# Kernel optimization log

Measured on AMD Instinct MI355X. Metric: run time of the kernel, lower is better.

## Reference

```python
import jax, jax.numpy as jnp
import numpy as np

NUM_HEADS = 8
EPS = 1e-12  # torch F.normalize default eps


def _l2norm(t):
    # t / max(||t||_2, eps) along last axis (matches F.normalize)
    n = jnp.sqrt(jnp.sum(t * t, axis=-1, keepdims=True))
    return t / jnp.maximum(n, EPS)


def setup_inputs() -> dict:
    key = jax.random.key(0)
    k1, k2, k3 = jax.random.split(key, 3)
    B, N, C = 8, 1024, 768
    x = jax.random.normal(k1, (B, N, C), dtype=jnp.float32)
    w_qkv = jax.random.normal(k2, (C, 3 * C), dtype=jnp.float32) * 0.02
    temperature = jnp.ones((NUM_HEADS, 1, 1), dtype=jnp.float32)
    w_proj = jax.random.normal(k3, (C, C), dtype=jnp.float32) * 0.02
    b_proj = jnp.zeros((C,), dtype=jnp.float32)
    return {"x": x, "w_qkv": w_qkv, "temperature": temperature,
            "w_proj": w_proj, "b_proj": b_proj}


def reference(x, w_qkv, temperature, w_proj, b_proj):
    B, N, C = x.shape
    H = NUM_HEADS
    hd = C // H
    # qkv projection (no bias), split into q,k,v of shape [B,H,N,hd]
    qkv = (x @ w_qkv).reshape(B, N, 3, H, hd)
    qkv = jnp.transpose(qkv, (2, 0, 3, 1, 4))  # [3,B,H,N,hd]
    q, k, v = qkv[0], qkv[1], qkv[2]
    q = _l2norm(q)
    k = _l2norm(k)
    # NOTE: code (unlike canonical XCA) does NOT transpose q/k, so attn is [B,H,N,N]
    attn = jnp.einsum('bhnd,bhmd->bhnm', q, k) * temperature  # temp broadcasts over B
    attn = jax.nn.softmax(attn, axis=-1)
    out = jnp.einsum('bhnm,bhmd->bhnd', attn, v)  # [B,H,N,hd]
    out = jnp.transpose(out, (0, 2, 1, 3)).reshape(B, N, C)
    return out @ w_proj + b_proj
```

## Files before the change

### kernel.cpp

```cpp
#include <hip/hip_runtime.h>
#include <math.h>

typedef __attribute__((ext_vector_type(8))) short bf16x8;
typedef __attribute__((ext_vector_type(4))) float f32x4;
typedef __attribute__((ext_vector_type(4))) unsigned int u32x4;
typedef unsigned short u16;
typedef unsigned int u32;


__device__ __forceinline__ u16 f2b(float f) {
  u32 u = __float_as_uint(f);
  return (u16)((u + 0x7fffu + ((u >> 16) & 1u)) >> 16);
}
__device__ __forceinline__ float b2f(u16 h) {
  return __uint_as_float(((u32)h) << 16);
}
__device__ __forceinline__ int swz(int m) { return (m ^ (m >> 2)) & 3; }

__device__ __forceinline__ void async16(const void* g, void* l) {
  __builtin_amdgcn_global_load_lds((const __attribute__((address_space(1))) u32*)g,
                                   (__attribute__((address_space(3))) u32*)l, 16, 0, 0);
}

template<int N> __device__ __forceinline__ void wait_vmcnt();
template<> __device__ __forceinline__ void wait_vmcnt<0>() {
  asm volatile("s_waitcnt vmcnt(0)" ::: "memory");
}
template<> __device__ __forceinline__ void wait_vmcnt<3>() {
  asm volatile("s_waitcnt vmcnt(3)" ::: "memory");
}

__global__ __launch_bounds__(256) void prep_kernel(const float* __restrict__ x,
                                                   const float* __restrict__ w_qkv,
                                                   const float* __restrict__ w_proj,
                                                   u16* __restrict__ xb,
                                                   u16* __restrict__ wqkvT,
                                                   u16* __restrict__ wprojT) {
  __shared__ float t[32][33];
  const int blk = blockIdx.x;
  if (blk < 6144) {
    const int idx = blk * 256 + threadIdx.x;
    const float4 v = ((const float4*)x)[idx];
    uint2 o;
    o.x = (u32)f2b(v.x) | ((u32)f2b(v.y) << 16);
    o.y = (u32)f2b(v.z) | ((u32)f2b(v.w) << 16);
    ((uint2*)xb)[idx] = o;
    return;
  }
  const float* in; u16* out; int R, C, bx, by;
  if (blk < 6144 + 1728) {
    const int rem = blk - 6144;
    in = w_qkv; out = wqkvT; R = 768; C = 2304; bx = rem % 72; by = rem / 72;
  } else {
    const int rem = blk - 6144 - 1728;
    in = w_proj; out = wprojT; R = 768; C = 768; bx = rem % 24; by = rem / 24;
  }
  const int c0 = bx * 32, r0 = by * 32;
  const int tc = threadIdx.x & 31, tr = threadIdx.x >> 5;
#pragma unroll
  for (int j = 0; j < 4; ++j)
    t[tr + j * 8][tc] = in[(size_t)(r0 + tr + j * 8) * C + c0 + tc];
  __syncthreads();
#pragma unroll
  for (int j = 0; j < 4; ++j)
    out[(size_t)(c0 + tr + j * 8) * R + r0 + tc] = f2b(t[tc][tr + j * 8]);
}

template<int NT>
__device__ __forceinline__ void gemm_core_bk64(const u16* __restrict__ A,
                                               const u16* __restrict__ Bt,
                                               int m0, int n0, f32x4 acc[4][NT / 32]) {
  constexpr int JT = NT / 32;
  constexpr int NG = (128 + NT) * 8;
  constexpr int NINST = NG / 256;
  __shared__ u16 Sm[2 * NG * 8];
  const int tid = threadIdx.x;
  const int w = tid >> 6, lane = tid & 63;
  const int i15 = lane & 15, quad = lane >> 4;
  const int wm = (w >> 1) * 64, wn = (w & 1) * (NT / 2);
  const int sw = quad ^ swz(i15);
  const int par = i15 & 1;

#pragma unroll
  for (int i = 0; i < 4; ++i)
#pragma unroll
    for (int j = 0; j < JT; ++j) acc[i][j] = (f32x4){0.f, 0.f, 0.f, 0.f};

  const u16* gsrc[NINST];
#pragma unroll
  for (int inst = 0; inst < NINST; ++inst) {
    const int s = inst * 256 + tid;
    if (s < 1024) {
      const int m = s >> 3, hp = (s >> 2) & 1, qd = s & 3;
      const int e = (hp ^ (m & 1)) * 4 + (qd ^ swz(m));
      gsrc[inst] = A + ((size_t)(m0 + m) * 768 + e * 8);
    } else {
      const int s2 = s - 1024;
      const int n = s2 >> 3, hp = (s2 >> 2) & 1, qd = s2 & 3;
      const int e = (hp ^ (n & 1)) * 4 + (qd ^ swz(n));
      gsrc[inst] = Bt + ((size_t)(n0 + n) * 768 + e * 8);
    }
  }

  auto stage = [&](int bsel) {
#pragma unroll
    for (int inst = 0; inst < NINST; ++inst) {
      async16(gsrc[inst], (void*)(Sm + ((size_t)bsel * NG + inst * 256 + w * 64) * 8));
      gsrc[inst] += 64;
    }
  };

  stage(0);

  for (int t = 0; t < 12; ++t) {
    __syncthreads();
    if (t < 11) stage((t + 1) & 1);
    const u16* buf = Sm + (size_t)(t & 1) * NG * 8;
#pragma unroll
    for (int kk = 0; kk < 2; ++kk) {
      bf16x8 af[4], bf[JT];
#pragma unroll
      for (int i = 0; i < 4; ++i) {
        const int mh = wm + i * 16 + i15;
        af[i] = *(const bf16x8*)(buf + ((size_t)mh * 8 + ((kk ^ par) << 2) + sw) * 8);
      }
#pragma unroll
      for (int j = 0; j < JT; ++j) {
        const int nh = wn + j * 16 + i15;
        bf[j] = *(const bf16x8*)(buf + ((size_t)1024 + nh * 8 + ((kk ^ par) << 2) + sw) * 8);
      }
#pragma unroll
      for (int i = 0; i < 4; ++i)
#pragma unroll
        for (int j = 0; j < JT; ++j)
          acc[i][j] = __builtin_amdgcn_mfma_f32_16x16x32_bf16(af[i], bf[j], acc[i][j], 0, 0, 0);
    }
  }
}

template<int NT>
__device__ __forceinline__ void gemm_core_c3(const u16* __restrict__ A,
                                             const u16* __restrict__ Bt,
                                             int m0, int n0, f32x4 acc[4][NT / 32]) {
  constexpr int JT = NT / 32;
  constexpr int NG = 512 + NT * 4;
  constexpr int NINST = NG / 256;
  __shared__ u16 Sm[3 * NG * 8];
  const int tid = threadIdx.x;
  const int w = tid >> 6, lane = tid & 63;
  const int i15 = lane & 15, quad = lane >> 4;
  const int wm = (w >> 1) * 64, wn = (w & 1) * (NT / 2);
  const int sw = quad ^ swz(i15);

#pragma unroll
  for (int i = 0; i < 4; ++i)
#pragma unroll
    for (int j = 0; j < JT; ++j) acc[i][j] = (f32x4){0.f, 0.f, 0.f, 0.f};

  const u16* gsrc[NINST];
#pragma unroll
  for (int inst = 0; inst < NINST; ++inst) {
    const int s = inst * 256 + tid;
    if (s < 512) {
      const int m = s >> 2, e = s & 3;
      gsrc[inst] = A + ((size_t)(m0 + m) * 768 + (e ^ swz(m)) * 8);
    } else {
      const int s2 = s - 512;
      const int n = s2 >> 2, e = s2 & 3;
      gsrc[inst] = Bt + ((size_t)(n0 + n) * 768 + (e ^ swz(n)) * 8);
    }
  }

  auto stage = [&](int bsel) {
#pragma unroll
    for (int inst = 0; inst < NINST; ++inst) {
      async16(gsrc[inst], (void*)(Sm + ((size_t)bsel * NG + inst * 256 + w * 64) * 8));
      gsrc[inst] += 32;
    }
  };

  stage(0);
  stage(1);

  for (int t = 0; t < 24; ++t) {
    if (t < 23) wait_vmcnt<NINST>();
    else        wait_vmcnt<0>();
    __builtin_amdgcn_s_barrier();
    __builtin_amdgcn_sched_barrier(0);
    if (t < 22) stage((t + 2) % 3);
    const u16* buf = Sm + (size_t)(t % 3) * NG * 8;
    bf16x8 af[4], bf[JT];
#pragma unroll
    for (int i = 0; i < 4; ++i)
      af[i] = *(const bf16x8*)(buf + ((size_t)(wm + i * 16 + i15) * 4 + sw) * 8);
#pragma unroll
    for (int j = 0; j < JT; ++j)
      bf[j] = *(const bf16x8*)(buf + ((size_t)512 + (wn + j * 16 + i15) * 4 + sw) * 8);
#pragma unroll
    for (int i = 0; i < 4; ++i)
#pragma unroll
      for (int j = 0; j < JT; ++j)
        acc[i][j] = __builtin_amdgcn_mfma_f32_16x16x32_bf16(af[i], bf[j], acc[i][j], 0, 0, 0);
  }
}

__global__ __launch_bounds__(256, 2) void qkv_gemm_kernel(
    const u16* __restrict__ xb, const u16* __restrict__ wT,
    const float* __restrict__ temp,
    u16* __restrict__ q, u16* __restrict__ k, u16* __restrict__ vT) {
  f32x4 acc[4][6];
  const int bid = blockIdx.x;
  const int xcd = bid & 7, slot = bid >> 3;
  const int mb = xcd * 8 + slot / 12, nb = slot % 12;
  const int m0 = mb * 128, n0 = nb * 192;
  gemm_core_bk64<192>(xb, wT, m0, n0, acc);

  const int tid = threadIdx.x, w = tid >> 6, lane = tid & 63;
  const int i15 = lane & 15, quad = lane >> 4;
  const int wm = (w >> 1) * 64;
  const int three = nb >> 2;
  const int h = ((nb & 3) << 1) + (w & 1);

  if (three < 2) {
    u16* dst = three ? k : q;
    const float sc_extra = three ? 1.f : temp[h];
#pragma unroll
    for (int it = 0; it < 4; ++it) {
#pragma unroll
      for (int r = 0; r < 4; ++r) {
        float s = 0.f;
#pragma unroll
        for (int jt = 0; jt < 6; ++jt) s += acc[it][jt][r] * acc[it][jt][r];
        s += __shfl_xor(s, 1); s += __shfl_xor(s, 2);
        s += __shfl_xor(s, 4); s += __shfl_xor(s, 8);
        const float scale = sc_extra / fmaxf(sqrtf(s), 1e-12f);
        const int m = m0 + wm + it * 16 + quad * 4 + r;
        const int b = m >> 10, n = m & 1023;
        u16* rowp = dst + ((size_t)(b * 8 + h) * 1024 + n) * 96;
#pragma unroll
        for (int jt = 0; jt < 6; ++jt)
          rowp[jt * 16 + i15] = f2b(acc[it][jt][r] * scale);
      }
    }
  } else {
#pragma unroll
    for (int it = 0; it < 4; ++it) {
      const int mb4 = m0 + wm + it * 16 + quad * 4;
      const int b = mb4 >> 10, nbase = mb4 & 1023;
#pragma unroll
      for (int jt = 0; jt < 6; ++jt) {
        const int d = jt * 16 + i15;
        uint2 pk;
        pk.x = (u32)f2b(acc[it][jt][0]) | ((u32)f2b(acc[it][jt][1]) << 16);
        pk.y = (u32)f2b(acc[it][jt][2]) | ((u32)f2b(acc[it][jt][3]) << 16);
        *(uint2*)(vT + ((size_t)(b * 8 + h) * 96 + d) * 1024 + nbase) = pk;
      }
    }
  }
}

__global__ __launch_bounds__(512, 4) void attn_kernel(
    const u16* __restrict__ q, const u16* __restrict__ kk,
    const u16* __restrict__ vT, u16* __restrict__ ctx) {
  __shared__ u16 smem[32768];
  const int tid = threadIdx.x, w = tid >> 6, lane = tid & 63;
  const int i15 = lane & 15, quad = lane >> 4;
  const int xs = swz(i15);
  const int bh = blockIdx.x & 63, qbase = (blockIdx.x >> 6) * 128;
  const int b = bh >> 3, h = bh & 7;
  u16* Pw = smem + 24576 + w * 1024;

  bf16x8 qf[3];
  {
    const int qrow = qbase + w * 16 + i15;
    const u16* qp = q + ((size_t)bh * 1024 + qrow) * 96 + quad * 8;
#pragma unroll
    for (int c = 0; c < 3; ++c) qf[c] = *(const bf16x8*)(qp + c * 32);
  }

  const u16* gsrc[3]; int gstep[3];
#pragma unroll
  for (int inst = 0; inst < 3; ++inst) {
    const int s = inst * 512 + tid;
    if (s < 768) {
      const int key6 = (s & 255) >> 2, c = s >> 8;
      const int e = c * 4 + ((s & 3) ^ swz(key6));
      gsrc[inst] = kk + ((size_t)bh * 1024 + key6) * 96 + e * 8;
      gstep[inst] = 64 * 96;
    } else {
      const int s2 = s - 768, r = s2 >> 2;
      const int c2 = (r >= 96), d = r - 96 * c2;
      gsrc[inst] = vT + ((size_t)bh * 96 + d) * 1024 + c2 * 32 + ((s2 & 3) ^ swz(d)) * 8;
      gstep[inst] = 64;
    }
  }

#pragma unroll
  for (int inst = 0; inst < 3; ++inst)
    async16(gsrc[inst], (void*)(smem + (size_t)(inst * 512 + w * 64) * 8));

  f32x4 o[6];
#pragma unroll
  for (int dt = 0; dt < 6; ++dt) o[dt] = (f32x4){0.f, 0.f, 0.f, 0.f};
  float l = 0.f;

  for (int t = 0; t < 16; ++t) {
    __syncthreads();
    const u16* KVs = smem + (t & 1) * 12288;
    if (t < 15) {
      u16* dst = smem + ((t + 1) & 1) * 12288;
#pragma unroll
      for (int inst = 0; inst < 3; ++inst) {
        gsrc[inst] += gstep[inst];
        async16(gsrc[inst], (void*)(dst + (size_t)(inst * 512 + w * 64) * 8));
      }
    }
#pragma unroll
    for (int kt = 0; kt < 4; ++kt) {
      bf16x8 af[3];
#pragma unroll
      for (int c = 0; c < 3; ++c)
        af[c] = *(const bf16x8*)(KVs + ((size_t)((c * 64 + kt * 16 + i15) * 4) + (quad ^ xs)) * 8);
      f32x4 s = (f32x4){0.f, 0.f, 0.f, 0.f};
#pragma unroll
      for (int c = 0; c < 3; ++c)
        s = __builtin_amdgcn_mfma_f32_16x16x32_bf16(af[c], qf[c], s, 0, 0, 0);
      const float e0 = __expf(s[0]), e1 = __expf(s[1]);
      const float e2 = __expf(s[2]), e3 = __expf(s[3]);
      l += (e0 + e1) + (e2 + e3);
      uint2 pk;
      pk.x = (u32)f2b(e0) | ((u32)f2b(e1) << 16);
      pk.y = (u32)f2b(e2) | ((u32)f2b(e3) << 16);
      const int pg = (kt & 1) * 2 + (quad >> 1);
      *(uint2*)(Pw + (size_t)(((kt >> 1) * 16 + i15) * 4 + (pg ^ xs)) * 8
                    + (quad & 1) * 4) = pk;
    }
#pragma unroll
    for (int c2 = 0; c2 < 2; ++c2) {
      const bf16x8 pa = *(const bf16x8*)(Pw + (size_t)((c2 * 16 + i15) * 4 + (quad ^ xs)) * 8);
#pragma unroll
      for (int dt = 0; dt < 6; ++dt) {
        const bf16x8 vb = *(const bf16x8*)(KVs +
            ((size_t)(768 + (c2 * 96 + dt * 16 + i15) * 4) + (quad ^ xs)) * 8);
        o[dt] = __builtin_amdgcn_mfma_f32_16x16x32_bf16(pa, vb, o[dt], 0, 0, 0);
      }
    }
  }

  l += __shfl_xor(l, 16); l += __shfl_xor(l, 32);
  __syncthreads();
  u16* scr = smem + w * 1664;
#pragma unroll
  for (int r = 0; r < 4; ++r) {
    const float linv = 1.f / __shfl(l, quad * 4 + r);
    const int row16 = quad * 4 + r;
#pragma unroll
    for (int dt = 0; dt < 6; ++dt)
      scr[row16 * 104 + dt * 16 + i15] = f2b(o[dt][r] * linv);
  }
#pragma unroll
  for (int jj = 0; jj < 3; ++jj) {
    const int id = jj * 64 + lane;
    const int row16 = id / 12, g = id - row16 * 12;
    const int grow = b * 1024 + qbase + w * 16 + row16;
    *(uint4*)(ctx + (size_t)grow * 768 + h * 96 + g * 8) =
        *(const uint4*)(scr + row16 * 104 + g * 8);
  }
}

__global__ __launch_bounds__(256, 4) void proj_gemm_kernel(
    const u16* __restrict__ ctx, const u16* __restrict__ wT,
    const float* __restrict__ bias, float* __restrict__ out) {
  f32x4 acc[4][2];
  const int bid = blockIdx.x;
  const int xcd = bid & 7, slot = bid >> 3;
  const int mb = xcd * 8 + slot / 12, nb = slot % 12;
  const int m0 = mb * 128, n0 = nb * 64;
  gemm_core_c3<64>(ctx, wT, m0, n0, acc);

  const int tid = threadIdx.x, w = tid >> 6, lane = tid & 63;
  const int i15 = lane & 15, quad = lane >> 4;
  const int wm = (w >> 1) * 64, wn = (w & 1) * 32;
#pragma unroll
  for (int jt = 0; jt < 2; ++jt) {
    const int c = n0 + wn + jt * 16 + i15;
    const float bb = bias[c];
#pragma unroll
    for (int it = 0; it < 4; ++it) {
#pragma unroll
      for (int r = 0; r < 4; ++r) {
        const int m = m0 + wm + it * 16 + quad * 4 + r;
        out[(size_t)m * 768 + c] = acc[it][jt][r] + bb;
      }
    }
  }
}

extern "C" void kernel_launch(void* const* d_in, const int* in_sizes, int n_in,
                              void* d_out, int out_size, void* d_ws, size_t ws_size,
                              hipStream_t stream) {
  const float* x      = (const float*)d_in[0];
  const float* w_qkv  = (const float*)d_in[1];
  const float* temp   = (const float*)d_in[2];
  const float* w_proj = (const float*)d_in[3];
  const float* b_proj = (const float*)d_in[4];

  u16* ws      = (u16*)d_ws;
  u16* xb      = ws;
  u16* wqkvT   = xb + 6291456;
  u16* qb      = wqkvT + 1769472;
  u16* kb      = qb + 6291456;
  u16* vTb     = kb + 6291456;
  u16* ctxb    = vTb + 6291456;
  u16* wprojT  = ctxb + 6291456;

  prep_kernel<<<8448, 256, 0, stream>>>(x, w_qkv, w_proj, xb, wqkvT, wprojT);
  qkv_gemm_kernel<<<768, 256, 0, stream>>>(xb, wqkvT, temp, qb, kb, vTb);
  attn_kernel<<<512, 512, 0, stream>>>(qb, kb, vTb, ctxb);
  proj_gemm_kernel<<<768, 256, 0, stream>>>(ctxb, wprojT, b_proj, (float*)d_out);
}
```

Measured before the change: 178.3 us.

## Use single-buffered BK32 QKV GEMM, raise occupancy, add setprio and intrinsic bf16 convert

Replaces the double-buffered BK=64 QKV GEMM core with a single-buffered BK=32 loop that issues async loads and syncs twice per iteration. Launch bounds for the QKV kernel rise from 2 to 3 blocks per CU, trading software pipelining for more resident waves. The attention kernel wraps its MFMA groups in s_setprio and swaps the manual bf16 rounding for the HIP intrinsic conversion. Losing overlap of loads with MFMA inside a block may stall the GEMM unless the extra occupancy hides that latency.

```diff
diff --git a/kernel.cpp b/kernel.cpp
--- a/kernel.cpp
+++ b/kernel.cpp
@@ -1,4 +1,5 @@
 #include <hip/hip_runtime.h>
+#include <hip/hip_bf16.h>
 #include <math.h>
 
 typedef __attribute__((ext_vector_type(8))) short bf16x8;
@@ -11,6 +12,10 @@
 __device__ __forceinline__ u16 f2b(float f) {
   u32 u = __float_as_uint(f);
   return (u16)((u + 0x7fffu + ((u >> 16) & 1u)) >> 16);
+}
+__device__ __forceinline__ u16 f2bq(float f) {
+  __hip_bfloat16 h = __float2bfloat16(f);
+  return __bfloat16_as_ushort(h);
 }
 __device__ __forceinline__ float b2f(u16 h) {
   return __uint_as_float(((u32)h) << 16);
@@ -67,74 +72,52 @@
 }
 
 template<int NT>
-__device__ __forceinline__ void gemm_core_bk64(const u16* __restrict__ A,
-                                               const u16* __restrict__ Bt,
-                                               int m0, int n0, f32x4 acc[4][NT / 32]) {
+__device__ __forceinline__ void gemm_core2b(const u16* __restrict__ A,
+                                            const u16* __restrict__ Bt,
+                                            int m0, int n0, f32x4 acc[4][NT / 32]) {
   constexpr int JT = NT / 32;
-  constexpr int NG = (128 + NT) * 8;
-  constexpr int NINST = NG / 256;
-  __shared__ u16 Sm[2 * NG * 8];
+  constexpr int NINST = (512 + NT * 4) / 256;
+  __shared__ u16 Sm[(512 + NT * 4) * 8];
   const int tid = threadIdx.x;
   const int w = tid >> 6, lane = tid & 63;
   const int i15 = lane & 15, quad = lane >> 4;
   const int wm = (w >> 1) * 64, wn = (w & 1) * (NT / 2);
   const int sw = quad ^ swz(i15);
-  const int par = i15 & 1;
 
 #pragma unroll
   for (int i = 0; i < 4; ++i)
 #pragma unroll
     for (int j = 0; j < JT; ++j) acc[i][j] = (f32x4){0.f, 0.f, 0.f, 0.f};
 
-  const u16* gsrc[NINST];
-#pragma unroll
-  for (int inst = 0; inst < NINST; ++inst) {
-    const int s = inst * 256 + tid;
-    if (s < 1024) {
-      const int m = s >> 3, hp = (s >> 2) & 1, qd = s & 3;
-      const int e = (hp ^ (m & 1)) * 4 + (qd ^ swz(m));
-      gsrc[inst] = A + ((size_t)(m0 + m) * 768 + e * 8);
-    } else {
-      const int s2 = s - 1024;
-      const int n = s2 >> 3, hp = (s2 >> 2) & 1, qd = s2 & 3;
-      const int e = (hp ^ (n & 1)) * 4 + (qd ^ swz(n));
-      gsrc[inst] = Bt + ((size_t)(n0 + n) * 768 + e * 8);
-    }
-  }
-
-  auto stage = [&](int bsel) {
+  for (int k0 = 0; k0 < 768; k0 += 32) {
+    __syncthreads();
 #pragma unroll
     for (int inst = 0; inst < NINST; ++inst) {
-      async16(gsrc[inst], (void*)(Sm + ((size_t)bsel * NG + inst * 256 + w * 64) * 8));
-      gsrc[inst] += 64;
-    }
-  };
-
-  stage(0);
-
-  for (int t = 0; t < 12; ++t) {
+      const int s = inst * 256 + tid;
+      const u16* src;
+      if (inst < 2) {
+        const int m = s >> 2, e = s & 3;
+        src = A + ((size_t)(m0 + m) * 768 + k0 + (e ^ swz(m)) * 8);
+      } else {
+        const int s2 = s - 512;
+        const int n = s2 >> 2, e = s2 & 3;
+        src = Bt + ((size_t)(n0 + n) * 768 + k0 + (e ^ swz(n)) * 8);
+      }
+      async16(src, (void*)(Sm + (size_t)(inst * 256 + w * 64) * 8));
+    }
     __syncthreads();
-    if (t < 11) stage((t + 1) & 1);
-    const u16* buf = Sm + (size_t)(t & 1) * NG * 8;
-#pragma unroll
-    for (int kk = 0; kk < 2; ++kk) {
-      bf16x8 af[4], bf[JT];
-#pragma unroll
-      for (int i = 0; i < 4; ++i) {
-        const int mh = wm + i * 16 + i15;
-        af[i] = *(const bf16x8*)(buf + ((size_t)mh * 8 + ((kk ^ par) << 2) + sw) * 8);
-      }
-#pragma unroll
-      for (int j = 0; j < JT; ++j) {
-        const int nh = wn + j * 16 + i15;
-        bf[j] = *(const bf16x8*)(buf + ((size_t)1024 + nh * 8 + ((kk ^ par) << 2) + sw) * 8);
-      }
-#pragma unroll
-      for (int i = 0; i < 4; ++i)
-#pragma unroll
-        for (int j = 0; j < JT; ++j)
-          acc[i][j] = __builtin_amdgcn_mfma_f32_16x16x32_bf16(af[i], bf[j], acc[i][j], 0, 0, 0);
-    }
+    bf16x8 af[4], bf[JT];
+#pragma unroll
+    for (int i = 0; i < 4; ++i)
+      af[i] = *(const bf16x8*)(Sm + ((size_t)(wm + i * 16 + i15) * 4 + sw) * 8);
+#pragma unroll
+    for (int j = 0; j < JT; ++j)
+      bf[j] = *(const bf16x8*)(Sm + ((size_t)512 + (wn + j * 16 + i15) * 4 + sw) * 8);
+#pragma unroll
+    for (int i = 0; i < 4; ++i)
+#pragma unroll
+      for (int j = 0; j < JT; ++j)
+        acc[i][j] = __builtin_amdgcn_mfma_f32_16x16x32_bf16(af[i], bf[j], acc[i][j], 0, 0, 0);
   }
 }
 
@@ -204,7 +187,7 @@
   }
 }
 
-__global__ __launch_bounds__(256, 2) void qkv_gemm_kernel(
+__global__ __launch_bounds__(256, 3) void qkv_gemm_kernel(
     const u16* __restrict__ xb, const u16* __restrict__ wT,
     const float* __restrict__ temp,
     u16* __restrict__ q, u16* __restrict__ k, u16* __restrict__ vT) {
@@ -213,7 +196,7 @@
   const int xcd = bid & 7, slot = bid >> 3;
   const int mb = xcd * 8 + slot / 12, nb = slot % 12;
   const int m0 = mb * 128, n0 = nb * 192;
-  gemm_core_bk64<192>(xb, wT, m0, n0, acc);
+  gemm_core2b<192>(xb, wT, m0, n0, acc);
 
   const int tid = threadIdx.x, w = tid >> 6, lane = tid & 63;
   const int i15 = lane & 15, quad = lane >> 4;
@@ -322,15 +305,17 @@
       for (int c = 0; c < 3; ++c)
         af[c] = *(const bf16x8*)(KVs + ((size_t)((c * 64 + kt * 16 + i15) * 4) + (quad ^ xs)) * 8);
       f32x4 s = (f32x4){0.f, 0.f, 0.f, 0.f};
+      __builtin_amdgcn_s_setprio(1);
 #pragma unroll
       for (int c = 0; c < 3; ++c)
         s = __builtin_amdgcn_mfma_f32_16x16x32_bf16(af[c], qf[c], s, 0, 0, 0);
+      __builtin_amdgcn_s_setprio(0);
       const float e0 = __expf(s[0]), e1 = __expf(s[1]);
       const float e2 = __expf(s[2]), e3 = __expf(s[3]);
       l += (e0 + e1) + (e2 + e3);
       uint2 pk;
-      pk.x = (u32)f2b(e0) | ((u32)f2b(e1) << 16);
-      pk.y = (u32)f2b(e2) | ((u32)f2b(e3) << 16);
+      pk.x = (u32)f2bq(e0) | ((u32)f2bq(e1) << 16);
+      pk.y = (u32)f2bq(e2) | ((u32)f2bq(e3) << 16);
       const int pg = (kt & 1) * 2 + (quad >> 1);
       *(uint2*)(Pw + (size_t)(((kt >> 1) * 16 + i15) * 4 + (pg ^ xs)) * 8
                     + (quad & 1) * 4) = pk;
@@ -338,12 +323,14 @@
 #pragma unroll
     for (int c2 = 0; c2 < 2; ++c2) {
       const bf16x8 pa = *(const bf16x8*)(Pw + (size_t)((c2 * 16 + i15) * 4 + (quad ^ xs)) * 8);
+      __builtin_amdgcn_s_setprio(1);
 #pragma unroll
       for (int dt = 0; dt < 6; ++dt) {
         const bf16x8 vb = *(const bf16x8*)(KVs +
             ((size_t)(768 + (c2 * 96 + dt * 16 + i15) * 4) + (quad ^ xs)) * 8);
         o[dt] = __builtin_amdgcn_mfma_f32_16x16x32_bf16(pa, vb, o[dt], 0, 0, 0);
       }
+      __builtin_amdgcn_s_setprio(0);
     }
   }
 
@@ -356,7 +343,7 @@
     const int row16 = quad * 4 + r;
 #pragma unroll
     for (int dt = 0; dt < 6; ++dt)
-      scr[row16 * 104 + dt * 16 + i15] = f2b(o[dt][r] * linv);
+      scr[row16 * 104 + dt * 16 + i15] = f2bq(o[dt][r] * linv);
   }
 #pragma unroll
   for (int jj = 0; jj < 3; ++jj) {
```

After: 179.1 us. Within noise of the previous version (+0.5%).
